# Performance work log

Hardware: AMD Instinct MI355X
Metric: run time of the kernel (lower is better)

The kernel has to match this reference:

```python
import jax, jax.numpy as jnp
import numpy as np

LN_EPS = 1e-5
NEG_INF = -1e38


def wkv_scan(w, u, k, v):
    """Numerically-stable RWKV WKV recurrence (matches wkv_cuda forward).
    w: [C] (negative decay), u: [C] bonus, k/v: [B,T,C]. Returns y: [B,T,C]."""
    Bdim, T, C = k.shape

    def step(carry, kv_t):
        p, q, o = carry  # running num, den, log-scale, each [B,C]
        kt, vt = kv_t
        no = jnp.maximum(o, u + kt)
        A = jnp.exp(o - no)
        Bw = jnp.exp(u + kt - no)
        y = (A * p + Bw * vt) / (A * q + Bw)
        no2 = jnp.maximum(w + o, kt)
        A2 = jnp.exp(w + o - no2)
        B2 = jnp.exp(kt - no2)
        return (A2 * p + B2 * vt, A2 * q + B2, no2), y

    init = (jnp.zeros((Bdim, C), k.dtype), jnp.zeros((Bdim, C), k.dtype),
            jnp.full((Bdim, C), NEG_INF, k.dtype))
    kT = jnp.moveaxis(k, 1, 0)  # [T,B,C]
    vT = jnp.moveaxis(v, 1, 0)
    _, ys = jax.lax.scan(step, init, (kT, vT))
    return jnp.moveaxis(ys, 0, 1)  # [B,T,C]


def setup_inputs() -> dict:
    key = jax.random.key(0)
    ks = jax.random.split(key, 8)
    B, C, H, W = 16, 192, 56, 56
    s = 0.02
    x = jax.random.normal(ks[0], (B, C, H, W), jnp.float32)
    Wk = jax.random.normal(ks[1], (C, C), jnp.float32) * s
    Wv = jax.random.normal(ks[2], (C, C), jnp.float32) * s
    Wr = jax.random.normal(ks[3], (C, C), jnp.float32) * s
    Wo = jax.random.normal(ks[4], (C, C), jnp.float32) * s
    ln_g = jnp.ones((C,), jnp.float32)
    ln_b = jnp.zeros((C,), jnp.float32)
    w_decay = -6.0 + 0.1 * jax.random.normal(ks[5], (C,), jnp.float32)
    u = 0.1 * jax.random.normal(ks[6], (C,), jnp.float32)
    return {"x": x, "Wk": Wk, "Wv": Wv, "Wr": Wr, "Wo": Wo,
            "ln_g": ln_g, "ln_b": ln_b, "w_decay": w_decay, "u": u}


def reference(x, Wk, Wv, Wr, Wo, ln_g, ln_b, w_decay, u):
    B, C, H, W = x.shape
    xs = jnp.transpose(x.reshape(B, C, H * W), (0, 2, 1))  # [B,T,C]
    k = jnp.einsum('btc,dc->btd', xs, Wk)
    v = jnp.einsum('btc,dc->btd', xs, Wv)
    r = jnp.einsum('btc,dc->btd', xs, Wr)
    real_w = -jnp.exp(w_decay)
    x_fwd = wkv_scan(real_w, u, k, v)
    x_bwd = jnp.flip(wkv_scan(real_w, u, jnp.flip(k, 1), jnp.flip(v, 1)), 1)
    x_bi = 0.5 * (x_fwd + x_bwd)
    h = jax.nn.sigmoid(r) * x_bi
    mu = jnp.mean(h, axis=-1, keepdims=True)
    var = jnp.var(h, axis=-1, keepdims=True)
    h = (h - mu) * jax.lax.rsqrt(var + LN_EPS) * ln_g + ln_b
    out = jnp.einsum('btc,dc->btd', h, Wo)  # dropout is identity at eval
    return jnp.transpose(out, (0, 2, 1)).reshape(B, C, H, W)
```

## Files before the change

kernel.cpp:

```cpp
#include <hip/hip_runtime.h>
#include <hip/hip_bf16.h>

#define BB 16
#define CC 192
#define TPIX 3136
#define NCH 49
#define CHL 64
#define NNELE ((size_t)BB * TPIX * CC)
#define NSTATE ((size_t)2 * BB * NCH * CC)
#define WCH (CC * CC)

typedef __attribute__((ext_vector_type(8))) short bf16x8;
typedef __attribute__((ext_vector_type(4))) float f32x4;
typedef __attribute__((ext_vector_type(16))) float f32x16;

__device__ __forceinline__ unsigned short f2bf(float f) {
    __hip_bfloat16 b = __float2bfloat16(f);
    return *reinterpret_cast<unsigned short*>(&b);
}
__device__ __forceinline__ float bf2f(unsigned short h) {
    union { unsigned u; float f; } v; v.u = ((unsigned)h) << 16;
    return v.f;
}


__global__ __launch_bounds__(256) void wcvt_frag(
    const float* __restrict__ Wk, const float* __restrict__ Wv,
    const float* __restrict__ Wr, const float* __restrict__ Wo,
    unsigned short* __restrict__ wfrag)
{
    const int id = blockIdx.x * 256 + threadIdx.x;
    const int m = id / 4608;
    const int r = id % 4608;
    const int tile = r >> 6;
    const int lane = r & 63;
    const int dr = tile / 12, tk = tile % 12;
    const int d = dr * 32 + (lane & 31);
    const int c = tk * 16 + (lane >> 5) * 8;
    const float* W = (m == 0) ? Wk : (m == 1) ? Wv : (m == 2) ? Wr : Wo;
    const float4 a = *(const float4*)&W[d * CC + c];
    const float4 b = *(const float4*)&W[d * CC + c + 4];
    bf16x8 o;
    o[0] = (short)f2bf(a.x); o[1] = (short)f2bf(a.y);
    o[2] = (short)f2bf(a.z); o[3] = (short)f2bf(a.w);
    o[4] = (short)f2bf(b.x); o[5] = (short)f2bf(b.y);
    o[6] = (short)f2bf(b.z); o[7] = (short)f2bf(b.w);
    *(bf16x8*)&wfrag[(size_t)m * WCH + (size_t)tile * 512 + lane * 8] = o;
}

__global__ __launch_bounds__(256) void xcvt_frag(
    const float* __restrict__ x, unsigned short* __restrict__ xfrag)
{
    const int t0 = blockIdx.x * 32;
    const int b  = blockIdx.y;
    __shared__ float ls[CC][33];
    const int tid = threadIdx.x;
#pragma unroll
    for (int it = 0; it < 6; ++it) {
        const int c  = it * 32 + (tid >> 3);
        const int t4 = (tid & 7) * 4;
        *(float4*)&ls[c][t4] =
            *(const float4*)&x[((size_t)b * CC + c) * TPIX + t0 + t4];
    }
    __syncthreads();
    const size_t tbase = ((size_t)(b * TPIX + t0) >> 5) * 12;
#pragma unroll
    for (int it = 0; it < 3; ++it) {
        const int id = it * 256 + tid;
        const int tk = id >> 6;
        const int lane = id & 63;
        const int r32 = lane & 31;
        const int c0 = tk * 16 + (lane >> 5) * 8;
        bf16x8 o;
#pragma unroll
        for (int e = 0; e < 8; ++e)
            o[e] = (short)f2bf(ls[c0 + e][r32]);
        *(bf16x8*)&xfrag[(tbase + tk) * 512 + lane * 8] = o;
    }
}

__global__ __launch_bounds__(512, 4) void proj_mfma32(
    const unsigned short* __restrict__ xfrag,
    const unsigned short* __restrict__ wfrag,
    unsigned short* __restrict__ kbf, unsigned short* __restrict__ vbf,
    unsigned short* __restrict__ rfrag)
{
    __shared__ unsigned short wlds[WCH];
    const int tid  = threadIdx.x;
    const int lane = tid & 63;
    const int wv   = tid >> 6;
    const int tw   = wv >> 1;
    const int dwav = wv & 1;
    const int l31  = lane & 31;
    const int kh   = lane >> 5;
    const int m    = blockIdx.z;

    const size_t row0 = (size_t)blockIdx.x * 128 + tw * 32;
    const size_t xtb  = (row0 >> 5) * 12;

    bf16x8 xf[12];
#pragma unroll
    for (int ks = 0; ks < 12; ++ks)
        xf[ks] = *(const bf16x8*)&xfrag[(xtb + ks) * 512 + lane * 8];

    const unsigned short* wm = wfrag + (size_t)m * WCH;
#pragma unroll
    for (int it = 0; it < 9; ++it) {
        const int off = (it * 512 + tid) * 8;
        *(bf16x8*)&wlds[off] = *(const bf16x8*)&wm[off];
    }
    __syncthreads();

    f32x16 acc[3];
#pragma unroll
    for (int nn = 0; nn < 3; ++nn)
#pragma unroll
        for (int e = 0; e < 16; ++e) acc[nn][e] = 0.f;

#pragma unroll
    for (int ks = 0; ks < 12; ++ks) {
        bf16x8 wf[3];
#pragma unroll
        for (int nn = 0; nn < 3; ++nn)
            wf[nn] = *(const bf16x8*)&wlds[((dwav * 3 + nn) * 12 + ks) * 512 + lane * 8];
#pragma unroll
        for (int nn = 0; nn < 3; ++nn)
            acc[nn] = __builtin_amdgcn_mfma_f32_32x32x16_bf16(
                xf[ks], wf[nn], acc[nn], 0, 0, 0);
    }

    if (m == 2) {
#pragma unroll
        for (int nn = 0; nn < 3; ++nn) {
            const int d = dwav * 96 + nn * 32 + l31;
            const size_t tb = ((row0 >> 5) * 12 + (d >> 4)) * 512 +
                              (size_t)(((d >> 3) & 1) * 32) * 8 + (d & 7);
#pragma unroll
            for (int q = 0; q < 16; ++q) {
                const int tq = (q & 3) + 8 * (q >> 2) + 4 * kh;
                rfrag[tb + tq * 8] = f2bf(acc[nn][q]);
            }
        }
    } else {
        unsigned short* om = (m == 0) ? kbf : vbf;
#pragma unroll
        for (int nn = 0; nn < 3; ++nn) {
            const int d = dwav * 96 + nn * 32 + l31;
#pragma unroll
            for (int q = 0; q < 16; ++q) {
                const int t = (q & 3) + 8 * (q >> 2) + 4 * kh;
                om[(row0 + t) * CC + d] = f2bf(acc[nn][q]);
            }
        }
    }
}

__global__ __launch_bounds__(256) void wkv_chunk_kernel(
    const unsigned short* __restrict__ kb, const unsigned short* __restrict__ vb,
    const float* __restrict__ wdec,
    float* __restrict__ sp, float* __restrict__ sq, float* __restrict__ so)
{
    const int gid = blockIdx.x * 256 + threadIdx.x;
    const int c  = gid % CC;
    const int r  = gid / CC;
    const int ch = r % NCH;
    const int r2 = r / NCH;
    const int b  = r2 % BB;
    const int dir = r2 / BB;

    const float w = -__expf(wdec[c]);
    const int tstart = dir ? (TPIX - 1 - ch * CHL) : (ch * CHL);
    const long stride = dir ? -(long)CC : (long)CC;
    long idx = ((long)b * TPIX + tstart) * CC + c;

    float p = 0.f, q = 0.f, o = -1e38f;
#pragma unroll 4
    for (int j = 0; j < CHL; ++j) {
        const float kt = bf2f(kb[idx]), vt = bf2f(vb[idx]);
        const float wo  = w + o;
        const float no2 = fmaxf(wo, kt);
        const float A2  = __expf(wo - no2);
        const float B2  = __expf(kt - no2);
        p = A2 * p + B2 * vt;
        q = A2 * q + B2;
        o = no2;
        idx += stride;
    }
    sp[gid] = p; sq[gid] = q; so[gid] = o;
}

__global__ __launch_bounds__(256) void wkv_prefix_kernel(
    float* __restrict__ sp, float* __restrict__ sq, float* __restrict__ so,
    const float* __restrict__ wdec)
{
    const int tid = blockIdx.x * 256 + threadIdx.x;
    if (tid >= 2 * BB * CC) return;
    const int c = tid % CC;
    const int g = tid / CC;
    const float w  = -__expf(wdec[c]);
    const float wL = w * CHL;

    float P = 0.f, Q = 0.f, O = -1e38f;
    size_t idx = (size_t)g * NCH * CC + c;
    for (int ch = 0; ch < NCH; ++ch) {
        const float pl = sp[idx], ql = sq[idx], ol = so[idx];
        sp[idx] = P; sq[idx] = Q; so[idx] = O;
        const float Ow = O + wL;
        const float no = fmaxf(Ow, ol);
        const float A  = __expf(Ow - no);
        const float Bf = __expf(ol - no);
        P = A * P + Bf * pl;
        Q = A * Q + Bf * ql;
        O = no;
        idx += CC;
    }
}

__global__ __launch_bounds__(256) void wkv_emit_kernel(
    const unsigned short* __restrict__ kb, const unsigned short* __restrict__ vb,
    const float* __restrict__ wdec, const float* __restrict__ ubias,
    const float* __restrict__ sp, const float* __restrict__ sq,
    const float* __restrict__ so,
    unsigned short* __restrict__ yfwd, unsigned short* __restrict__ ybwd)
{
    const int gid = blockIdx.x * 256 + threadIdx.x;
    const int c  = gid % CC;
    const int r  = gid / CC;
    const int ch = r % NCH;
    const int r2 = r / NCH;
    const int b  = r2 % BB;
    const int dir = r2 / BB;

    const float w = -__expf(wdec[c]);
    const float u = ubias[c];
    const int tstart = dir ? (TPIX - 1 - ch * CHL) : (ch * CHL);
    const long stride = dir ? -(long)CC : (long)CC;
    const int rstep = dir ? -1 : 1;
    long idx = ((long)b * TPIX + tstart) * CC + c;
    long row = (long)b * TPIX + tstart;
    unsigned short* yout = dir ? ybwd : yfwd;
    const int ctile = c >> 4;
    const int clane = ((c >> 3) & 1) * 32;
    const int ce    = c & 7;

    float p = sp[gid], q = sq[gid], o = so[gid];
#pragma unroll 2
    for (int j = 0; j < CHL; ++j) {
        const float kt = bf2f(kb[idx]), vt = bf2f(vb[idx]);
        const float uk  = u + kt;
        const float no  = fmaxf(o, uk);
        const float A   = __expf(o - no);
        const float Bw  = __expf(uk - no);
        const float num = A * p + Bw * vt;
        const float den = A * q + Bw;
        const size_t off = ((size_t)(row >> 5) * 12 + ctile) * 512 +
                           (size_t)((row & 31) + clane) * 8 + ce;
        yout[off] = f2bf(0.5f * __fdividef(num, den));
        const float wo  = w + o;
        const float no2 = fmaxf(wo, kt);
        const float A2  = __expf(wo - no2);
        const float B2  = __expf(kt - no2);
        p = A2 * p + B2 * vt;
        q = A2 * q + B2;
        o = no2;
        idx += stride;
        row += rstep;
    }
}

__global__ __launch_bounds__(512) void outproj_ln_mfma32(
    const unsigned short* __restrict__ yfwd, const unsigned short* __restrict__ ybwd,
    const unsigned short* __restrict__ rfrag,
    const float* __restrict__ gamma, const float* __restrict__ beta,
    const unsigned short* __restrict__ wo,
    float* __restrict__ out)
{
    __shared__ unsigned short wlds[WCH];
    __shared__ float gblds[CC];
    __shared__ float bblds[CC];
    const int tid  = threadIdx.x;
    const int lane = tid & 63;
    const int wv   = tid >> 6;
    const int tw   = wv >> 1;
    const int dwav = wv & 1;
    const int l31  = lane & 31;
    const int kh   = lane >> 5;

#pragma unroll
    for (int it = 0; it < 9; ++it) {
        const int off = (it * 512 + tid) * 8;
        *(bf16x8*)&wlds[off] = *(const bf16x8*)&wo[off];
    }
    if (tid < CC) { gblds[tid] = gamma[tid]; bblds[tid] = beta[tid]; }
    __syncthreads();

    const size_t row0 = (size_t)blockIdx.x * 128 + tw * 32;
    const size_t htb  = (row0 >> 5) * 12;

    bf16x8 hvb[12];
    float s = 0.f, s2 = 0.f;
#pragma unroll
    for (int ks = 0; ks < 12; ++ks) {
        const size_t fo = (htb + ks) * 512 + lane * 8;
        const bf16x8 yf = *(const bf16x8*)&yfwd[fo];
        const bf16x8 yb = *(const bf16x8*)&ybwd[fo];
        const bf16x8 rv = *(const bf16x8*)&rfrag[fo];
        bf16x8 hb;
#pragma unroll
        for (int e = 0; e < 8; ++e) {
            const float xb = bf2f((unsigned short)yf[e]) + bf2f((unsigned short)yb[e]);
            const float rr = bf2f((unsigned short)rv[e]);
            const float h  = xb / (1.f + __expf(-rr));
            s += h; s2 += h * h;
            hb[e] = (short)f2bf(h);
        }
        hvb[ks] = hb;
    }
    s  += __shfl_xor(s, 32);
    s2 += __shfl_xor(s2, 32);
    const float mu   = s * (1.f / CC);
    const float var  = s2 * (1.f / CC) - mu * mu;
    const float rstd = rsqrtf(var + 1e-5f);

#pragma unroll
    for (int ks = 0; ks < 12; ++ks) {
        const int cbase = ks * 16 + kh * 8;
        const f32x4 g0 = *(const f32x4*)&gblds[cbase];
        const f32x4 g1 = *(const f32x4*)&gblds[cbase + 4];
        const f32x4 b0 = *(const f32x4*)&bblds[cbase];
        const f32x4 b1 = *(const f32x4*)&bblds[cbase + 4];
        bf16x8 hb = hvb[ks];
#pragma unroll
        for (int e = 0; e < 4; ++e) {
            const float h0 = (bf2f((unsigned short)hb[e]) - mu) * rstd * g0[e] + b0[e];
            const float h1 = (bf2f((unsigned short)hb[e + 4]) - mu) * rstd * g1[e] + b1[e];
            hb[e]     = (short)f2bf(h0);
            hb[e + 4] = (short)f2bf(h1);
        }
        hvb[ks] = hb;
    }

    f32x16 acc[3];
#pragma unroll
    for (int nn = 0; nn < 3; ++nn)
#pragma unroll
        for (int e = 0; e < 16; ++e) acc[nn][e] = 0.f;

#pragma unroll
    for (int ks = 0; ks < 12; ++ks) {
        bf16x8 wf[3];
#pragma unroll
        for (int nn = 0; nn < 3; ++nn)
            wf[nn] = *(const bf16x8*)&wlds[((dwav * 3 + nn) * 12 + ks) * 512 + lane * 8];
#pragma unroll
        for (int nn = 0; nn < 3; ++nn)
            acc[nn] = __builtin_amdgcn_mfma_f32_32x32x16_bf16(
                hvb[ks], wf[nn], acc[nn], 0, 0, 0);
    }

#pragma unroll
    for (int nn = 0; nn < 3; ++nn) {
        const int d = dwav * 96 + nn * 32 + l31;
#pragma unroll
        for (int q2 = 0; q2 < 4; ++q2) {
            const size_t grow = row0 + 4 * kh + 8 * q2;
            const int b  = (int)(grow / TPIX);
            const int tl = (int)(grow % TPIX);
            f32x4 v4 = {acc[nn][q2 * 4 + 0], acc[nn][q2 * 4 + 1],
                        acc[nn][q2 * 4 + 2], acc[nn][q2 * 4 + 3]};
            *(f32x4*)&out[((size_t)b * CC + d) * TPIX + tl] = v4;
        }
    }
}

extern "C" void kernel_launch(void* const* d_in, const int* in_sizes, int n_in,
                              void* d_out, int out_size, void* d_ws, size_t ws_size,
                              hipStream_t stream)
{
    const float* x    = (const float*)d_in[0];
    const float* Wk   = (const float*)d_in[1];
    const float* Wv   = (const float*)d_in[2];
    const float* Wr   = (const float*)d_in[3];
    const float* Wo   = (const float*)d_in[4];
    const float* ln_g = (const float*)d_in[5];
    const float* ln_b = (const float*)d_in[6];
    const float* wdec = (const float*)d_in[7];
    const float* u    = (const float*)d_in[8];

    unsigned short* kbf   = (unsigned short*)d_ws;
    unsigned short* vbf   = kbf + NNELE;
    unsigned short* rfrag = vbf + NNELE;
    unsigned short* xfrag = rfrag + NNELE;
    unsigned short* wfrag = xfrag + NNELE;
    unsigned short* yfwd  = wfrag + 4 * WCH;
    unsigned short* ybwd  = yfwd + NNELE;
    float* sp = (float*)xfrag;
    float* sq = sp + NSTATE;
    float* so = sq + NSTATE;
    float* out = (float*)d_out;

    wcvt_frag<<<72, 256, 0, stream>>>(Wk, Wv, Wr, Wo, wfrag);
    xcvt_frag<<<dim3(TPIX / 32, BB), 256, 0, stream>>>(x, xfrag);

    proj_mfma32<<<dim3((BB * TPIX) / 128, 1, 3), 512, 0, stream>>>(
        xfrag, wfrag, kbf, vbf, rfrag);

    const int nth = (int)NSTATE;
    wkv_chunk_kernel<<<nth / 256, 256, 0, stream>>>(kbf, vbf, wdec, sp, sq, so);
    wkv_prefix_kernel<<<(2 * BB * CC + 255) / 256, 256, 0, stream>>>(sp, sq, so, wdec);
    wkv_emit_kernel<<<nth / 256, 256, 0, stream>>>(kbf, vbf, wdec, u, sp, sq, so, yfwd, ybwd);

    outproj_ln_mfma32<<<(BB * TPIX) / 128, 512, 0, stream>>>(
        yfwd, ybwd, rfrag, ln_g, ln_b, wfrag + 3 * WCH, out);
}
```

Before: 131.9 us.

## Recompute gated activations in outproj pass to cut registers and raise occupancy

```diff
diff --git a/kernel.cpp b/kernel.cpp
--- a/kernel.cpp
+++ b/kernel.cpp
@@ -268,7 +268,7 @@
     }
 }
 
-__global__ __launch_bounds__(512) void outproj_ln_mfma32(
+__global__ __launch_bounds__(512, 2) void outproj_ln_mfma32(
     const unsigned short* __restrict__ yfwd, const unsigned short* __restrict__ ybwd,
     const unsigned short* __restrict__ rfrag,
     const float* __restrict__ gamma, const float* __restrict__ beta,
@@ -286,18 +286,9 @@
     const int l31  = lane & 31;
     const int kh   = lane >> 5;
 
-#pragma unroll
-    for (int it = 0; it < 9; ++it) {
-        const int off = (it * 512 + tid) * 8;
-        *(bf16x8*)&wlds[off] = *(const bf16x8*)&wo[off];
-    }
-    if (tid < CC) { gblds[tid] = gamma[tid]; bblds[tid] = beta[tid]; }
-    __syncthreads();
-
     const size_t row0 = (size_t)blockIdx.x * 128 + tw * 32;
     const size_t htb  = (row0 >> 5) * 12;
 
-    bf16x8 hvb[12];
     float s = 0.f, s2 = 0.f;
 #pragma unroll
     for (int ks = 0; ks < 12; ++ks) {
@@ -305,49 +296,56 @@
         const bf16x8 yf = *(const bf16x8*)&yfwd[fo];
         const bf16x8 yb = *(const bf16x8*)&ybwd[fo];
         const bf16x8 rv = *(const bf16x8*)&rfrag[fo];
-        bf16x8 hb;
 #pragma unroll
         for (int e = 0; e < 8; ++e) {
             const float xb = bf2f((unsigned short)yf[e]) + bf2f((unsigned short)yb[e]);
             const float rr = bf2f((unsigned short)rv[e]);
             const float h  = xb / (1.f + __expf(-rr));
             s += h; s2 += h * h;
-            hb[e] = (short)f2bf(h);
-        }
-        hvb[ks] = hb;
-    }
+        }
+    }
+
+#pragma unroll
+    for (int it = 0; it < 9; ++it) {
+        const int off = (it * 512 + tid) * 8;
+        *(bf16x8*)&wlds[off] = *(const bf16x8*)&wo[off];
+    }
+    if (tid < CC) { gblds[tid] = gamma[tid]; bblds[tid] = beta[tid]; }
+
     s  += __shfl_xor(s, 32);
     s2 += __shfl_xor(s2, 32);
     const float mu   = s * (1.f / CC);
     const float var  = s2 * (1.f / CC) - mu * mu;
     const float rstd = rsqrtf(var + 1e-5f);
-
+    __syncthreads();
+
+    f32x16 acc[3];
+#pragma unroll
+    for (int nn = 0; nn < 3; ++nn)
+#pragma unroll
+        for (int e = 0; e < 16; ++e) acc[nn][e] = 0.f;
+
+    bf16x8 yf = *(const bf16x8*)&yfwd[htb * 512 + lane * 8];
+    bf16x8 yb = *(const bf16x8*)&ybwd[htb * 512 + lane * 8];
+    bf16x8 rv = *(const bf16x8*)&rfrag[htb * 512 + lane * 8];
 #pragma unroll
     for (int ks = 0; ks < 12; ++ks) {
+        bf16x8 nyf, nyb, nrv;
+        if (ks < 11) {
+            const size_t fo = (htb + ks + 1) * 512 + lane * 8;
+            nyf = *(const bf16x8*)&yfwd[fo];
+            nyb = *(const bf16x8*)&ybwd[fo];
+            nrv = *(const bf16x8*)&rfrag[fo];
+        }
         const int cbase = ks * 16 + kh * 8;
-        const f32x4 g0 = *(const f32x4*)&gblds[cbase];
-        const f32x4 g1 = *(const f32x4*)&gblds[cbase + 4];
-        const f32x4 b0 = *(const f32x4*)&bblds[cbase];
-        const f32x4 b1 = *(const f32x4*)&bblds[cbase + 4];
-        bf16x8 hb = hvb[ks];
-#pragma unroll
-        for (int e = 0; e < 4; ++e) {
-            const float h0 = (bf2f((unsigned short)hb[e]) - mu) * rstd * g0[e] + b0[e];
-            const float h1 = (bf2f((unsigned short)hb[e + 4]) - mu) * rstd * g1[e] + b1[e];
-            hb[e]     = (short)f2bf(h0);
-            hb[e + 4] = (short)f2bf(h1);
-        }
-        hvb[ks] = hb;
-    }
-
-    f32x16 acc[3];
-#pragma unroll
-    for (int nn = 0; nn < 3; ++nn)
-#pragma unroll
-        for (int e = 0; e < 16; ++e) acc[nn][e] = 0.f;
-
-#pragma unroll
-    for (int ks = 0; ks < 12; ++ks) {
+        bf16x8 hb;
+#pragma unroll
+        for (int e = 0; e < 8; ++e) {
+            const float xb = bf2f((unsigned short)yf[e]) + bf2f((unsigned short)yb[e]);
+            const float rr = bf2f((unsigned short)rv[e]);
+            const float h  = xb / (1.f + __expf(-rr));
+            hb[e] = (short)f2bf((h - mu) * rstd * gblds[cbase + e] + bblds[cbase + e]);
+        }
         bf16x8 wf[3];
 #pragma unroll
         for (int nn = 0; nn < 3; ++nn)
@@ -355,7 +353,8 @@
 #pragma unroll
         for (int nn = 0; nn < 3; ++nn)
             acc[nn] = __builtin_amdgcn_mfma_f32_32x32x16_bf16(
-                hvb[ks], wf[nn], acc[nn], 0, 0, 0);
+                hb, wf[nn], acc[nn], 0, 0, 0);
+        if (ks < 11) { yf = nyf; yb = nyb; rv = nrv; }
     }
 
 #pragma unroll
```

After: 147.7 us. 1.12x slower.
